# Kernel tuning notes

Hardware: AMD Instinct MI355X
Metric: run time of the kernel (lower is better)

## Reference

```python
import jax, jax.numpy as jnp
import numpy as np

B = 256       # number of grasp centers (batch)
N = 65536     # total points output by the backbone
C = 1024      # backbone feature channels (enc_channels[-1])
K = 512       # padded slots per segment (points per center)
INFO = 3      # info_size
KCLS = 6      # k_cls
EPS = 1e-5    # LayerNorm eps


def _layernorm(x, g, b):
    m = x.mean(-1, keepdims=True)
    v = ((x - m) ** 2).mean(-1, keepdims=True)
    return (x - m) / jnp.sqrt(v + EPS) * g + b


def setup_inputs() -> dict:
    key = jax.random.key(0)
    ks = jax.random.split(key, 10)
    feat = jax.random.normal(ks[0], (N, C), jnp.float32)
    offsets = jnp.sort(jax.random.randint(ks[1], (B,), 0, N)).astype(jnp.int64)
    offsets = offsets.at[-1].set(N)  # cumulative ends, last covers all points
    info = jax.random.normal(ks[2], (B, INFO), jnp.float32)

    def lin(k, o, i):
        return 0.02 * jax.random.normal(k, (o, i), jnp.float32), jnp.zeros((o,), jnp.float32)

    W1, b1 = lin(ks[3], 512, C)          # point_layer Linear(1024,512)
    Wi, bi = lin(ks[4], 32, INFO)        # info_layer Linear(info_size,32)
    Wa1, ba1 = lin(ks[5], 256, 544)      # anchor_mlp Linear(544,256)
    Wa2, ba2 = lin(ks[6], KCLS, 256)     # anchor_mlp Linear(256,k_cls)
    Wo1, bo1 = lin(ks[7], 256, 544)      # offset_mlp Linear(544,256)
    Wo2, bo2 = lin(ks[8], KCLS * 3, 256) # offset_mlp Linear(256,k_cls*3)
    return dict(
        feat=feat, info=info, offsets=offsets,
        W1=W1, b1=b1, ln1_g=jnp.ones((512,)), ln1_b=jnp.zeros((512,)),
        Wi=Wi, bi=bi,
        Wa1=Wa1, ba1=ba1, lna_g=jnp.ones((256,)), lna_b=jnp.zeros((256,)),
        Wa2=Wa2, ba2=ba2,
        Wo1=Wo1, bo1=bo1, lno_g=jnp.ones((256,)), lno_b=jnp.zeros((256,)),
        Wo2=Wo2, bo2=bo2,
    )


def reference(feat, info, W1, b1, ln1_g, ln1_b, Wi, bi,
              Wa1, ba1, lna_g, lna_b, Wa2, ba2,
              Wo1, bo1, lno_g, lno_b, Wo2, bo2, offsets):
    # --- fused segment-max replaces the pad loop + max over padded dim ---
    # point i belongs to segment b s.t. offsets[b-1] <= i < offsets[b]
    ids = jnp.searchsorted(offsets, jnp.arange(feat.shape[0]), side='right')
    segmax = jax.ops.segment_max(feat, ids, num_segments=B)  # (B, C)
    lengths = jnp.diff(offsets, prepend=0)
    # original zero-pads to K slots: segments shorter than K see 0 in the max
    features = jnp.where((lengths < K)[:, None], jnp.maximum(segmax, 0.0), segmax)

    # point_layer: Linear -> LayerNorm -> Dropout(eval: identity) -> ReLU
    pf = jax.nn.relu(_layernorm(features @ W1.T + b1, ln1_g, ln1_b))
    # info_layer
    inf = info @ Wi.T + bi
    x = jnp.concatenate([pf, inf], axis=1)  # (B, 544)

    pred = jax.nn.relu(_layernorm(x @ Wa1.T + ba1, lna_g, lna_b)) @ Wa2.T + ba2
    off = jax.nn.relu(_layernorm(x @ Wo1.T + bo1, lno_g, lno_b)) @ Wo2.T + bo2
    offset = off.reshape(-1, KCLS, 3)
    return features, pred, offset
```

## Files before the change

kernel.cpp:

```cpp
#include <hip/hip_runtime.h>
#include <cstdint>

#define NPTS 65536
#define CCH  1024
#define BSEG 256
#define KSLOT 512
#define WROWS 32

typedef float v4f __attribute__((ext_vector_type(4)));

__device__ __forceinline__ unsigned ukey(float f) {
  int i = __float_as_int(f);
  return i >= 0 ? ((unsigned)i | 0x80000000u) : ~(unsigned)i;
}
__device__ __forceinline__ float udec(unsigned u, bool rl) {
  float v;
  if (u >= 0x80000000u) v = __int_as_float((int)(u & 0x7FFFFFFFu));
  else                  v = __int_as_float((int)~u);
  if (u == 0u) v = -__builtin_inff();
  if (rl) v = fmaxf(v, 0.0f);
  return v;
}
__device__ __forceinline__ v4f vmax4(v4f a, v4f b) {
  v4f r;
  r.x = fmaxf(a.x, b.x); r.y = fmaxf(a.y, b.y);
  r.z = fmaxf(a.z, b.z); r.w = fmaxf(a.w, b.w);
  return r;
}

__global__ __launch_bounds__(256) void segmax_k(const float* __restrict__ feat,
                                                const int* __restrict__ offsets,
                                                unsigned* __restrict__ keys) {
  int t = threadIdx.x;
  int col = t << 2;
  int row0 = blockIdx.x * WROWS;
  int row_end = row0 + WROWS;
  int lo = 0, hi = BSEG - 1;
  while (lo < hi) { int mid = (lo + hi) >> 1; if (offsets[mid] > row0) hi = mid; else lo = mid + 1; }
  int seg = lo;
  int end = offsets[seg];
  const float NI = -__builtin_inff();
  v4f m; m.x = NI; m.y = NI; m.z = NI; m.w = NI;
  bool dirty = false;
  int r = row0;
  while (r < row_end) {
    while (r >= end) {
      if (dirty) {
        unsigned* kp = keys + (size_t)seg * CCH + col;
        atomicMax(kp + 0, ukey(m.x));
        atomicMax(kp + 1, ukey(m.y));
        atomicMax(kp + 2, ukey(m.z));
        atomicMax(kp + 3, ukey(m.w));
        m.x = NI; m.y = NI; m.z = NI; m.w = NI;
        dirty = false;
      }
      ++seg;
      end = offsets[seg];
    }
    int stop = min(row_end, end);
    const float* p = feat + (size_t)r * CCH + col;
    for (; r + 8 <= stop; r += 8) {
      v4f v[8];
#pragma unroll
      for (int j = 0; j < 8; ++j) v[j] = *(const v4f*)(p + (size_t)j * CCH);
      p += 8 * CCH;
#pragma unroll
      for (int d = 4; d; d >>= 1)
#pragma unroll
        for (int j = 0; j < d; ++j) v[j] = vmax4(v[j], v[j + d]);
      m = vmax4(m, v[0]);
    }
    for (; r < stop; ++r) {
      v4f v = *(const v4f*)(p);
      p += CCH;
      m = vmax4(m, v);
    }
    dirty = true;
  }
  if (dirty) {
    unsigned* kp = keys + (size_t)seg * CCH + col;
    atomicMax(kp + 0, ukey(m.x));
    atomicMax(kp + 1, ukey(m.y));
    atomicMax(kp + 2, ukey(m.z));
    atomicMax(kp + 3, ukey(m.w));
  }
}

__global__ __launch_bounds__(256) void gemm1_fused(
    const unsigned* __restrict__ keys, const int* __restrict__ offsets,
    const float* __restrict__ W1, float* __restrict__ features,
    float* __restrict__ part1) {
  __shared__ float As[32][68];
  __shared__ float Ws[32][68];
  int bx = blockIdx.x, by = blockIdx.y, bz = blockIdx.z;
  int t = threadIdx.x;
  int tx = t & 15, ty = t >> 4;
  int lr = t >> 3;
  int lk = (t & 7) << 2;
  int row0 = by * 64 + lr, row1 = row0 + 32;
  int len0 = offsets[row0] - (row0 ? offsets[row0 - 1] : 0);
  int len1 = offsets[row1] - offsets[row1 - 1];
  bool rl0 = len0 < KSLOT, rl1 = len1 < KSLOT;
  const unsigned* K0 = keys + (size_t)row0 * CCH + lk;
  const unsigned* K1 = keys + (size_t)row1 * CCH + lk;
  int c0 = bx * 64 + lr, c1 = c0 + 32;
  const float* Wr0 = W1 + (size_t)c0 * CCH + lk;
  const float* Wr1 = W1 + (size_t)c1 * CCH + lk;
  float acc[4][4] = {};
  for (int s = 0; s < 4; ++s) {
    int k0 = (bz * 4 + s) << 5;
    uint4 ua = *(const uint4*)(K0 + k0);
    uint4 ub = *(const uint4*)(K1 + k0);
    float4 w0 = *(const float4*)(Wr0 + k0);
    float4 w1 = *(const float4*)(Wr1 + k0);
    float4 a0 = make_float4(udec(ua.x, rl0), udec(ua.y, rl0), udec(ua.z, rl0), udec(ua.w, rl0));
    float4 a1 = make_float4(udec(ub.x, rl1), udec(ub.y, rl1), udec(ub.z, rl1), udec(ub.w, rl1));
    if (bx == 0) {
      *(float4*)(features + (size_t)row0 * CCH + k0 + lk) = a0;
      *(float4*)(features + (size_t)row1 * CCH + k0 + lk) = a1;
    }
    __syncthreads();
    As[lk + 0][lr] = a0.x; As[lk + 1][lr] = a0.y; As[lk + 2][lr] = a0.z; As[lk + 3][lr] = a0.w;
    As[lk + 0][lr + 32] = a1.x; As[lk + 1][lr + 32] = a1.y; As[lk + 2][lr + 32] = a1.z; As[lk + 3][lr + 32] = a1.w;
    Ws[lk + 0][lr] = w0.x; Ws[lk + 1][lr] = w0.y; Ws[lk + 2][lr] = w0.z; Ws[lk + 3][lr] = w0.w;
    Ws[lk + 0][lr + 32] = w1.x; Ws[lk + 1][lr + 32] = w1.y; Ws[lk + 2][lr + 32] = w1.z; Ws[lk + 3][lr + 32] = w1.w;
    __syncthreads();
#pragma unroll
    for (int kk = 0; kk < 32; ++kk) {
      float4 av = *(const float4*)&As[kk][ty << 2];
      float4 wv = *(const float4*)&Ws[kk][tx << 2];
      acc[0][0] += av.x * wv.x; acc[0][1] += av.x * wv.y; acc[0][2] += av.x * wv.z; acc[0][3] += av.x * wv.w;
      acc[1][0] += av.y * wv.x; acc[1][1] += av.y * wv.y; acc[1][2] += av.y * wv.z; acc[1][3] += av.y * wv.w;
      acc[2][0] += av.z * wv.x; acc[2][1] += av.z * wv.y; acc[2][2] += av.z * wv.z; acc[2][3] += av.z * wv.w;
      acc[3][0] += av.w * wv.x; acc[3][1] += av.w * wv.y; acc[3][2] += av.w * wv.z; acc[3][3] += av.w * wv.w;
    }
  }
  float* op = part1 + (size_t)bz * 131072 + (size_t)(by * 64 + (ty << 2)) * 512 + bx * 64 + (tx << 2);
#pragma unroll
  for (int i = 0; i < 4; ++i)
    *(float4*)(op + (size_t)i * 512) = make_float4(acc[i][0], acc[i][1], acc[i][2], acc[i][3]);
}

__global__ __launch_bounds__(256) void ln1_x_k(
    const float* __restrict__ part1, const float* __restrict__ b1,
    const float* __restrict__ g, const float* __restrict__ be,
    const float* __restrict__ info, const float* __restrict__ Wi, const float* __restrict__ bi,
    float* __restrict__ x) {
  int b = blockIdx.x, t = threadIdx.x;
  int wv = t >> 6, ln = t & 63;
  __shared__ float red[2][4];
  __shared__ float stats[2];
  const float* p = part1 + (size_t)b * 512;
  float z0 = b1[t], z1 = b1[t + 256];
#pragma unroll
  for (int j = 0; j < 8; ++j) {
    z0 += p[(size_t)j * 131072 + t];
    z1 += p[(size_t)j * 131072 + 256 + t];
  }
  float s = z0 + z1, q = z0 * z0 + z1 * z1;
#pragma unroll
  for (int o = 32; o; o >>= 1) { s += __shfl_down(s, o); q += __shfl_down(q, o); }
  if (ln == 0) { red[0][wv] = s; red[1][wv] = q; }
  __syncthreads();
  if (t == 0) {
    float S = red[0][0] + red[0][1] + red[0][2] + red[0][3];
    float Q = red[1][0] + red[1][1] + red[1][2] + red[1][3];
    float mean = S * (1.f / 512.f);
    float var = Q * (1.f / 512.f) - mean * mean;
    stats[0] = mean; stats[1] = rsqrtf(var + 1e-5f);
  }
  __syncthreads();
  float mean = stats[0], rstd = stats[1];
  x[b * 544 + t]       = fmaxf((z0 - mean) * rstd * g[t]       + be[t],       0.f);
  x[b * 544 + t + 256] = fmaxf((z1 - mean) * rstd * g[t + 256] + be[t + 256], 0.f);
  if (t < 32) {
    float i0 = info[b * 3], i1 = info[b * 3 + 1], i2 = info[b * 3 + 2];
    x[b * 544 + 512 + t] = bi[t] + Wi[t * 3] * i0 + Wi[t * 3 + 1] * i1 + Wi[t * 3 + 2] * i2;
  }
}

__global__ __launch_bounds__(256) void gemm_nt_part(
    const float* __restrict__ A, int lda,
    const float* __restrict__ Wlo, const float* __restrict__ Whi, int nlo, int ldw,
    float* __restrict__ part, int Ktot, int steps_per_chunk) {
  __shared__ float As[32][68];
  __shared__ float Ws[32][68];
  int bx = blockIdx.x, by = blockIdx.y, bz = blockIdx.z;
  int t = threadIdx.x;
  int tx = t & 15, ty = t >> 4;
  int steps_total = Ktot >> 5;
  int step0 = bz * steps_per_chunk;
  int nsteps = min(steps_per_chunk, steps_total - step0);
  int lr = t >> 3;
  int lk = (t & 7) << 2;
  const float* Arow0 = A + (size_t)(by * 64 + lr) * lda + lk;
  const float* Arow1 = Arow0 + (size_t)32 * lda;
  int c0 = bx * 64 + lr;
  int c1 = c0 + 32;
  const float* Wrow0 = (c0 < nlo ? Wlo + (size_t)c0 * ldw : Whi + (size_t)(c0 - nlo) * ldw) + lk;
  const float* Wrow1 = (c1 < nlo ? Wlo + (size_t)c1 * ldw : Whi + (size_t)(c1 - nlo) * ldw) + lk;
  float acc[4][4] = {};
  for (int s = 0; s < nsteps; ++s) {
    int k0 = (step0 + s) << 5;
    float4 a0 = *(const float4*)(Arow0 + k0);
    float4 a1 = *(const float4*)(Arow1 + k0);
    float4 w0 = *(const float4*)(Wrow0 + k0);
    float4 w1 = *(const float4*)(Wrow1 + k0);
    __syncthreads();
    As[lk + 0][lr] = a0.x; As[lk + 1][lr] = a0.y; As[lk + 2][lr] = a0.z; As[lk + 3][lr] = a0.w;
    As[lk + 0][lr + 32] = a1.x; As[lk + 1][lr + 32] = a1.y; As[lk + 2][lr + 32] = a1.z; As[lk + 3][lr + 32] = a1.w;
    Ws[lk + 0][lr] = w0.x; Ws[lk + 1][lr] = w0.y; Ws[lk + 2][lr] = w0.z; Ws[lk + 3][lr] = w0.w;
    Ws[lk + 0][lr + 32] = w1.x; Ws[lk + 1][lr + 32] = w1.y; Ws[lk + 2][lr + 32] = w1.z; Ws[lk + 3][lr + 32] = w1.w;
    __syncthreads();
#pragma unroll
    for (int kk = 0; kk < 32; ++kk) {
      float4 av = *(const float4*)&As[kk][ty << 2];
      float4 wv = *(const float4*)&Ws[kk][tx << 2];
      acc[0][0] += av.x * wv.x; acc[0][1] += av.x * wv.y; acc[0][2] += av.x * wv.z; acc[0][3] += av.x * wv.w;
      acc[1][0] += av.y * wv.x; acc[1][1] += av.y * wv.y; acc[1][2] += av.y * wv.z; acc[1][3] += av.y * wv.w;
      acc[2][0] += av.z * wv.x; acc[2][1] += av.z * wv.y; acc[2][2] += av.z * wv.z; acc[2][3] += av.z * wv.w;
      acc[3][0] += av.w * wv.x; acc[3][1] += av.w * wv.y; acc[3][2] += av.w * wv.z; acc[3][3] += av.w * wv.w;
    }
  }
  float* op = part + (size_t)bz * 131072 + (size_t)(by * 64 + (ty << 2)) * 512 + bx * 64 + (tx << 2);
#pragma unroll
  for (int i = 0; i < 4; ++i)
    *(float4*)(op + (size_t)i * 512) = make_float4(acc[i][0], acc[i][1], acc[i][2], acc[i][3]);
}

__global__ __launch_bounds__(256) void heads_k(
    const float* __restrict__ part2,
    const float* __restrict__ ba1, const float* __restrict__ ga, const float* __restrict__ bea,
    const float* __restrict__ Wa2, const float* __restrict__ ba2,
    const float* __restrict__ bo1, const float* __restrict__ go, const float* __restrict__ beo,
    const float* __restrict__ Wo2, const float* __restrict__ bo2,
    float* __restrict__ outp) {
  int b = blockIdx.x, t = threadIdx.x;
  int wv = t >> 6, ln = t & 63;
  __shared__ float h[512];
  __shared__ float red[4][4];
  __shared__ float stats[4];
  const float* p0 = part2 + (size_t)b * 512;
  float za = ba1[t], zo = bo1[t];
#pragma unroll
  for (int j = 0; j < 4; ++j) {
    za += p0[(size_t)j * 131072 + t];
    zo += p0[(size_t)j * 131072 + 256 + t];
  }
  float sa = za, qa = za * za, so = zo, qo = zo * zo;
#pragma unroll
  for (int o = 32; o; o >>= 1) {
    sa += __shfl_down(sa, o); qa += __shfl_down(qa, o);
    so += __shfl_down(so, o); qo += __shfl_down(qo, o);
  }
  if (ln == 0) { red[wv][0] = sa; red[wv][1] = qa; red[wv][2] = so; red[wv][3] = qo; }
  __syncthreads();
  if (t == 0) {
    float Sa = red[0][0] + red[1][0] + red[2][0] + red[3][0];
    float Qa = red[0][1] + red[1][1] + red[2][1] + red[3][1];
    float So = red[0][2] + red[1][2] + red[2][2] + red[3][2];
    float Qo = red[0][3] + red[1][3] + red[2][3] + red[3][3];
    float ma = Sa * (1.f / 256.f), va = Qa * (1.f / 256.f) - ma * ma;
    float mo = So * (1.f / 256.f), vo = Qo * (1.f / 256.f) - mo * mo;
    stats[0] = ma; stats[1] = rsqrtf(va + 1e-5f);
    stats[2] = mo; stats[3] = rsqrtf(vo + 1e-5f);
  }
  __syncthreads();
  h[t]       = fmaxf((za - stats[0]) * stats[1] * ga[t] + bea[t], 0.f);
  h[256 + t] = fmaxf((zo - stats[2]) * stats[3] * go[t] + beo[t], 0.f);
  __syncthreads();
  const float* hh = (wv == 0) ? h : (h + 256);
  const float* W2 = (wv == 0) ? Wa2 : Wo2;
  const float* b2 = (wv == 0) ? ba2 : bo2;
  int o0 = (wv == 0) ? 0 : (wv - 1) * 6;
  int base = (wv == 0) ? (262144 + b * 6) : (263680 + b * 18);
  float h0 = hh[ln], h1 = hh[64 + ln], h2v = hh[128 + ln], h3 = hh[192 + ln];
#pragma unroll
  for (int oo = 0; oo < 6; ++oo) {
    int o = o0 + oo;
    const float* w = W2 + o * 256;
    float pr = h0 * w[ln] + h1 * w[64 + ln] + h2v * w[128 + ln] + h3 * w[192 + ln];
#pragma unroll
    for (int d = 32; d; d >>= 1) pr += __shfl_down(pr, d);
    if (ln == 0) outp[base + o] = pr + b2[o];
  }
}

extern "C" void kernel_launch(void* const* d_in, const int* in_sizes, int n_in,
                              void* d_out, int out_size, void* d_ws, size_t ws_size,
                              hipStream_t stream) {
  const float* feat   = (const float*)d_in[0];
  const float* info   = (const float*)d_in[1];
  const int*   offs   = (const int*)d_in[2];
  const float* W1     = (const float*)d_in[3];
  const float* b1     = (const float*)d_in[4];
  const float* ln1_g  = (const float*)d_in[5];
  const float* ln1_b  = (const float*)d_in[6];
  const float* Wi     = (const float*)d_in[7];
  const float* bi     = (const float*)d_in[8];
  const float* Wa1    = (const float*)d_in[9];
  const float* ba1    = (const float*)d_in[10];
  const float* lna_g  = (const float*)d_in[11];
  const float* lna_b  = (const float*)d_in[12];
  const float* Wa2    = (const float*)d_in[13];
  const float* ba2    = (const float*)d_in[14];
  const float* Wo1    = (const float*)d_in[15];
  const float* bo1    = (const float*)d_in[16];
  const float* lno_g  = (const float*)d_in[17];
  const float* lno_b  = (const float*)d_in[18];
  const float* Wo2    = (const float*)d_in[19];
  const float* bo2    = (const float*)d_in[20];

  char* ws = (char*)d_ws;
  float*    part1 = (float*)ws;
  float*    part2 = (float*)(ws + (4u << 20));
  float*    xbuf  = (float*)(ws + (6u << 20));
  unsigned* keys  = (unsigned*)(ws + (7u << 20));
  float* features = (float*)d_out;
  float* outp     = (float*)d_out;

  hipMemsetAsync(keys, 0, (size_t)BSEG * CCH * sizeof(unsigned), stream);
  segmax_k<<<dim3(NPTS / WROWS), dim3(256), 0, stream>>>(feat, offs, keys);
  gemm1_fused<<<dim3(8, 4, 8), dim3(256), 0, stream>>>(keys, offs, W1, features, part1);
  ln1_x_k<<<dim3(256), dim3(256), 0, stream>>>(part1, b1, ln1_g, ln1_b, info, Wi, bi, xbuf);
  gemm_nt_part<<<dim3(8, 4, 4), dim3(256), 0, stream>>>(
      xbuf, 544, Wa1, Wo1, 256, 544, part2, 544, 5);
  heads_k<<<dim3(256), dim3(256), 0, stream>>>(
      part2, ba1, lna_g, lna_b, Wa2, ba2, bo1, lno_g, lno_b, Wo2, bo2, outp);
}
```

Before: 91.96 us.

## Fuse LayerNorm and head kernels into GEMMs via per-row-group grid barriers

Merges the LN1+info kernel into the first split-K GEMM and the heads kernel into the second GEMM. Each group of blocks sharing a row tile syncs through an atomic counter spin-barrier before reducing the split-K partials. This removes two kernel launches and their gaps. The barrier only works if all blocks in a group are co-resident (256 and 128 blocks, which is likely fine on this GPU), and the counters are zeroed by extending the existing memset.

```diff
diff --git a/kernel.cpp b/kernel.cpp
--- a/kernel.cpp
+++ b/kernel.cpp
@@ -26,6 +26,18 @@
   r.x = fmaxf(a.x, b.x); r.y = fmaxf(a.y, b.y);
   r.z = fmaxf(a.z, b.z); r.w = fmaxf(a.w, b.w);
   return r;
+}
+
+__device__ __forceinline__ void group_barrier(int* cnt, int expected, int t) {
+  __syncthreads();
+  if (t == 0) {
+    __threadfence();
+    atomicAdd(cnt, 1);
+    while (__hip_atomic_load(cnt, __ATOMIC_ACQUIRE, __HIP_MEMORY_SCOPE_AGENT) < expected)
+      __builtin_amdgcn_s_sleep(1);
+  }
+  __syncthreads();
+  __threadfence();
 }
 
 __global__ __launch_bounds__(256) void segmax_k(const float* __restrict__ feat,
@@ -89,9 +101,14 @@
 __global__ __launch_bounds__(256) void gemm1_fused(
     const unsigned* __restrict__ keys, const int* __restrict__ offsets,
     const float* __restrict__ W1, float* __restrict__ features,
-    float* __restrict__ part1) {
+    float* __restrict__ part1, int* __restrict__ cnt,
+    const float* __restrict__ b1, const float* __restrict__ g1, const float* __restrict__ be1,
+    const float* __restrict__ info, const float* __restrict__ Wi, const float* __restrict__ bi,
+    float* __restrict__ xbuf) {
   __shared__ float As[32][68];
   __shared__ float Ws[32][68];
+  __shared__ float red1[8];
+  __shared__ float st1[2];
   int bx = blockIdx.x, by = blockIdx.y, bz = blockIdx.z;
   int t = threadIdx.x;
   int tx = t & 15, ty = t >> 4;
@@ -139,66 +156,67 @@
 #pragma unroll
   for (int i = 0; i < 4; ++i)
     *(float4*)(op + (size_t)i * 512) = make_float4(acc[i][0], acc[i][1], acc[i][2], acc[i][3]);
-}
-
-__global__ __launch_bounds__(256) void ln1_x_k(
-    const float* __restrict__ part1, const float* __restrict__ b1,
-    const float* __restrict__ g, const float* __restrict__ be,
-    const float* __restrict__ info, const float* __restrict__ Wi, const float* __restrict__ bi,
-    float* __restrict__ x) {
-  int b = blockIdx.x, t = threadIdx.x;
-  int wv = t >> 6, ln = t & 63;
-  __shared__ float red[2][4];
-  __shared__ float stats[2];
-  const float* p = part1 + (size_t)b * 512;
-  float z0 = b1[t], z1 = b1[t + 256];
-#pragma unroll
-  for (int j = 0; j < 8; ++j) {
-    z0 += p[(size_t)j * 131072 + t];
-    z1 += p[(size_t)j * 131072 + 256 + t];
-  }
-  float s = z0 + z1, q = z0 * z0 + z1 * z1;
-#pragma unroll
-  for (int o = 32; o; o >>= 1) { s += __shfl_down(s, o); q += __shfl_down(q, o); }
-  if (ln == 0) { red[0][wv] = s; red[1][wv] = q; }
-  __syncthreads();
-  if (t == 0) {
-    float S = red[0][0] + red[0][1] + red[0][2] + red[0][3];
-    float Q = red[1][0] + red[1][1] + red[1][2] + red[1][3];
-    float mean = S * (1.f / 512.f);
-    float var = Q * (1.f / 512.f) - mean * mean;
-    stats[0] = mean; stats[1] = rsqrtf(var + 1e-5f);
-  }
-  __syncthreads();
-  float mean = stats[0], rstd = stats[1];
-  x[b * 544 + t]       = fmaxf((z0 - mean) * rstd * g[t]       + be[t],       0.f);
-  x[b * 544 + t + 256] = fmaxf((z1 - mean) * rstd * g[t + 256] + be[t + 256], 0.f);
-  if (t < 32) {
-    float i0 = info[b * 3], i1 = info[b * 3 + 1], i2 = info[b * 3 + 2];
-    x[b * 544 + 512 + t] = bi[t] + Wi[t * 3] * i0 + Wi[t * 3 + 1] * i1 + Wi[t * 3 + 2] * i2;
-  }
-}
-
-__global__ __launch_bounds__(256) void gemm_nt_part(
-    const float* __restrict__ A, int lda,
-    const float* __restrict__ Wlo, const float* __restrict__ Whi, int nlo, int ldw,
-    float* __restrict__ part, int Ktot, int steps_per_chunk) {
+
+  group_barrier(cnt + by, 64, t);
+  {
+    int r = by * 64 + (bx + 8 * bz);
+    int wv = t >> 6, ln = t & 63;
+    const float* p = part1 + (size_t)r * 512;
+    float z0 = b1[t], z1 = b1[t + 256];
+#pragma unroll
+    for (int j = 0; j < 8; ++j) {
+      z0 += p[(size_t)j * 131072 + t];
+      z1 += p[(size_t)j * 131072 + 256 + t];
+    }
+    float s = z0 + z1, q = z0 * z0 + z1 * z1;
+#pragma unroll
+    for (int o = 32; o; o >>= 1) { s += __shfl_down(s, o); q += __shfl_down(q, o); }
+    if (ln == 0) { red1[wv] = s; red1[4 + wv] = q; }
+    __syncthreads();
+    if (t == 0) {
+      float S = red1[0] + red1[1] + red1[2] + red1[3];
+      float Q = red1[4] + red1[5] + red1[6] + red1[7];
+      float mean = S * (1.f / 512.f);
+      float var = Q * (1.f / 512.f) - mean * mean;
+      st1[0] = mean; st1[1] = rsqrtf(var + 1e-5f);
+    }
+    __syncthreads();
+    float mean = st1[0], rstd = st1[1];
+    xbuf[r * 544 + t]       = fmaxf((z0 - mean) * rstd * g1[t]       + be1[t],       0.f);
+    xbuf[r * 544 + t + 256] = fmaxf((z1 - mean) * rstd * g1[t + 256] + be1[t + 256], 0.f);
+    if (t < 32) {
+      float i0 = info[r * 3], i1 = info[r * 3 + 1], i2 = info[r * 3 + 2];
+      xbuf[r * 544 + 512 + t] = bi[t] + Wi[t * 3] * i0 + Wi[t * 3 + 1] * i1 + Wi[t * 3 + 2] * i2;
+    }
+  }
+}
+
+__global__ __launch_bounds__(256) void gemm2_fused(
+    const float* __restrict__ A,
+    const float* __restrict__ Wa1, const float* __restrict__ Wo1,
+    float* __restrict__ part2, int* __restrict__ cnt,
+    const float* __restrict__ ba1, const float* __restrict__ ga, const float* __restrict__ bea,
+    const float* __restrict__ Wa2, const float* __restrict__ ba2,
+    const float* __restrict__ bo1, const float* __restrict__ go, const float* __restrict__ beo,
+    const float* __restrict__ Wo2, const float* __restrict__ bo2,
+    float* __restrict__ outp) {
   __shared__ float As[32][68];
   __shared__ float Ws[32][68];
+  __shared__ float hh[512];
+  __shared__ float red2[16];
+  __shared__ float st2[4];
   int bx = blockIdx.x, by = blockIdx.y, bz = blockIdx.z;
   int t = threadIdx.x;
   int tx = t & 15, ty = t >> 4;
-  int steps_total = Ktot >> 5;
-  int step0 = bz * steps_per_chunk;
-  int nsteps = min(steps_per_chunk, steps_total - step0);
+  int step0 = bz * 5;
+  int nsteps = min(5, 17 - step0);
   int lr = t >> 3;
   int lk = (t & 7) << 2;
-  const float* Arow0 = A + (size_t)(by * 64 + lr) * lda + lk;
-  const float* Arow1 = Arow0 + (size_t)32 * lda;
-  int c0 = bx * 64 + lr;
-  int c1 = c0 + 32;
-  const float* Wrow0 = (c0 < nlo ? Wlo + (size_t)c0 * ldw : Whi + (size_t)(c0 - nlo) * ldw) + lk;
-  const float* Wrow1 = (c1 < nlo ? Wlo + (size_t)c1 * ldw : Whi + (size_t)(c1 - nlo) * ldw) + lk;
+  const float* Arow0 = A + (size_t)(by * 64 + lr) * 544 + lk;
+  const float* Arow1 = Arow0 + (size_t)32 * 544;
+  int c0 = bx * 64 + lr, c1 = c0 + 32;
+  const float* Wrow0 = (c0 < 256 ? Wa1 + (size_t)c0 * 544 : Wo1 + (size_t)(c0 - 256) * 544) + lk;
+  const float* Wrow1 = (c1 < 256 ? Wa1 + (size_t)c1 * 544 : Wo1 + (size_t)(c1 - 256) * 544) + lk;
   float acc[4][4] = {};
   for (int s = 0; s < nsteps; ++s) {
     int k0 = (step0 + s) << 5;
@@ -222,67 +240,62 @@
       acc[3][0] += av.w * wv.x; acc[3][1] += av.w * wv.y; acc[3][2] += av.w * wv.z; acc[3][3] += av.w * wv.w;
     }
   }
-  float* op = part + (size_t)bz * 131072 + (size_t)(by * 64 + (ty << 2)) * 512 + bx * 64 + (tx << 2);
+  float* op = part2 + (size_t)bz * 131072 + (size_t)(by * 64 + (ty << 2)) * 512 + bx * 64 + (tx << 2);
 #pragma unroll
   for (int i = 0; i < 4; ++i)
     *(float4*)(op + (size_t)i * 512) = make_float4(acc[i][0], acc[i][1], acc[i][2], acc[i][3]);
-}
-
-__global__ __launch_bounds__(256) void heads_k(
-    const float* __restrict__ part2,
-    const float* __restrict__ ba1, const float* __restrict__ ga, const float* __restrict__ bea,
-    const float* __restrict__ Wa2, const float* __restrict__ ba2,
-    const float* __restrict__ bo1, const float* __restrict__ go, const float* __restrict__ beo,
-    const float* __restrict__ Wo2, const float* __restrict__ bo2,
-    float* __restrict__ outp) {
-  int b = blockIdx.x, t = threadIdx.x;
+
+  group_barrier(cnt + by, 32, t);
+  int gid = bx + 8 * bz;
   int wv = t >> 6, ln = t & 63;
-  __shared__ float h[512];
-  __shared__ float red[4][4];
-  __shared__ float stats[4];
-  const float* p0 = part2 + (size_t)b * 512;
-  float za = ba1[t], zo = bo1[t];
-#pragma unroll
-  for (int j = 0; j < 4; ++j) {
-    za += p0[(size_t)j * 131072 + t];
-    zo += p0[(size_t)j * 131072 + 256 + t];
-  }
-  float sa = za, qa = za * za, so = zo, qo = zo * zo;
-#pragma unroll
-  for (int o = 32; o; o >>= 1) {
-    sa += __shfl_down(sa, o); qa += __shfl_down(qa, o);
-    so += __shfl_down(so, o); qo += __shfl_down(qo, o);
-  }
-  if (ln == 0) { red[wv][0] = sa; red[wv][1] = qa; red[wv][2] = so; red[wv][3] = qo; }
-  __syncthreads();
-  if (t == 0) {
-    float Sa = red[0][0] + red[1][0] + red[2][0] + red[3][0];
-    float Qa = red[0][1] + red[1][1] + red[2][1] + red[3][1];
-    float So = red[0][2] + red[1][2] + red[2][2] + red[3][2];
-    float Qo = red[0][3] + red[1][3] + red[2][3] + red[3][3];
-    float ma = Sa * (1.f / 256.f), va = Qa * (1.f / 256.f) - ma * ma;
-    float mo = So * (1.f / 256.f), vo = Qo * (1.f / 256.f) - mo * mo;
-    stats[0] = ma; stats[1] = rsqrtf(va + 1e-5f);
-    stats[2] = mo; stats[3] = rsqrtf(vo + 1e-5f);
-  }
-  __syncthreads();
-  h[t]       = fmaxf((za - stats[0]) * stats[1] * ga[t] + bea[t], 0.f);
-  h[256 + t] = fmaxf((zo - stats[2]) * stats[3] * go[t] + beo[t], 0.f);
-  __syncthreads();
-  const float* hh = (wv == 0) ? h : (h + 256);
-  const float* W2 = (wv == 0) ? Wa2 : Wo2;
-  const float* b2 = (wv == 0) ? ba2 : bo2;
-  int o0 = (wv == 0) ? 0 : (wv - 1) * 6;
-  int base = (wv == 0) ? (262144 + b * 6) : (263680 + b * 18);
-  float h0 = hh[ln], h1 = hh[64 + ln], h2v = hh[128 + ln], h3 = hh[192 + ln];
-#pragma unroll
-  for (int oo = 0; oo < 6; ++oo) {
-    int o = o0 + oo;
-    const float* w = W2 + o * 256;
-    float pr = h0 * w[ln] + h1 * w[64 + ln] + h2v * w[128 + ln] + h3 * w[192 + ln];
-#pragma unroll
-    for (int d = 32; d; d >>= 1) pr += __shfl_down(pr, d);
-    if (ln == 0) outp[base + o] = pr + b2[o];
+#pragma unroll
+  for (int rr = 0; rr < 2; ++rr) {
+    int r = by * 64 + gid * 2 + rr;
+    const float* p0 = part2 + (size_t)r * 512;
+    float za = ba1[t], zo = bo1[t];
+#pragma unroll
+    for (int j = 0; j < 4; ++j) {
+      za += p0[(size_t)j * 131072 + t];
+      zo += p0[(size_t)j * 131072 + 256 + t];
+    }
+    float sa = za, qa = za * za, so = zo, qo = zo * zo;
+#pragma unroll
+    for (int o = 32; o; o >>= 1) {
+      sa += __shfl_down(sa, o); qa += __shfl_down(qa, o);
+      so += __shfl_down(so, o); qo += __shfl_down(qo, o);
+    }
+    if (ln == 0) { red2[wv] = sa; red2[4 + wv] = qa; red2[8 + wv] = so; red2[12 + wv] = qo; }
+    __syncthreads();
+    if (t == 0) {
+      float Sa = red2[0] + red2[1] + red2[2] + red2[3];
+      float Qa = red2[4] + red2[5] + red2[6] + red2[7];
+      float So = red2[8] + red2[9] + red2[10] + red2[11];
+      float Qo = red2[12] + red2[13] + red2[14] + red2[15];
+      float ma = Sa * (1.f / 256.f), va = Qa * (1.f / 256.f) - ma * ma;
+      float mo = So * (1.f / 256.f), vo = Qo * (1.f / 256.f) - mo * mo;
+      st2[0] = ma; st2[1] = rsqrtf(va + 1e-5f);
+      st2[2] = mo; st2[3] = rsqrtf(vo + 1e-5f);
+    }
+    __syncthreads();
+    hh[t]       = fmaxf((za - st2[0]) * st2[1] * ga[t] + bea[t], 0.f);
+    hh[256 + t] = fmaxf((zo - st2[2]) * st2[3] * go[t] + beo[t], 0.f);
+    __syncthreads();
+    const float* hp = (wv == 0) ? hh : (hh + 256);
+    const float* W2 = (wv == 0) ? Wa2 : Wo2;
+    const float* b2 = (wv == 0) ? ba2 : bo2;
+    int o0 = (wv == 0) ? 0 : (wv - 1) * 6;
+    int base = (wv == 0) ? (262144 + r * 6) : (263680 + r * 18);
+    float h0 = hp[ln], h1 = hp[64 + ln], h2v = hp[128 + ln], h3 = hp[192 + ln];
+#pragma unroll
+    for (int oo = 0; oo < 6; ++oo) {
+      int o = o0 + oo;
+      const float* w = W2 + o * 256;
+      float pr = h0 * w[ln] + h1 * w[64 + ln] + h2v * w[128 + ln] + h3 * w[192 + ln];
+#pragma unroll
+      for (int d = 32; d; d >>= 1) pr += __shfl_down(pr, d);
+      if (ln == 0) outp[base + o] = pr + b2[o];
+    }
+    __syncthreads();
   }
 }
 
@@ -316,15 +329,16 @@
   float*    part2 = (float*)(ws + (4u << 20));
   float*    xbuf  = (float*)(ws + (6u << 20));
   unsigned* keys  = (unsigned*)(ws + (7u << 20));
+  int*      cnts  = (int*)(ws + (8u << 20));
   float* features = (float*)d_out;
   float* outp     = (float*)d_out;
 
-  hipMemsetAsync(keys, 0, (size_t)BSEG * CCH * sizeof(unsigned), stream);
+  hipMemsetAsync(keys, 0, (size_t)BSEG * CCH * sizeof(unsigned) + 256, stream);
   segmax_k<<<dim3(NPTS / WROWS), dim3(256), 0, stream>>>(feat, offs, keys);
-  gemm1_fused<<<dim3(8, 4, 8), dim3(256), 0, stream>>>(keys, offs, W1, features, part1);
-  ln1_x_k<<<dim3(256), dim3(256), 0, stream>>>(part1, b1, ln1_g, ln1_b, info, Wi, bi, xbuf);
-  gemm_nt_part<<<dim3(8, 4, 4), dim3(256), 0, stream>>>(
-      xbuf, 544, Wa1, Wo1, 256, 544, part2, 544, 5);
-  heads_k<<<dim3(256), dim3(256), 0, stream>>>(
-      part2, ba1, lna_g, lna_b, Wa2, ba2, bo1, lno_g, lno_b, Wo2, bo2, outp);
-}
+  gemm1_fused<<<dim3(8, 4, 8), dim3(256), 0, stream>>>(
+      keys, offs, W1, features, part1, cnts,
+      b1, ln1_g, ln1_b, info, Wi, bi, xbuf);
+  gemm2_fused<<<dim3(8, 4, 4), dim3(256), 0, stream>>>(
+      xbuf, Wa1, Wo1, part2, cnts + 4,
+      ba1, lna_g, lna_b, Wa2, ba2, bo1, lno_g, lno_b, Wo2, bo2, outp);
+}
```

Measured after the change: 145.0 us. 57.7% more time.
